# Kernel optimization log

Measured on AMD Instinct MI355X. Metric: run time of the kernel, lower is better.

## Reference

```python
import jax, jax.numpy as jnp
import numpy as np

N = 50000
NEG_SLOPE = 0.2


def add_self_loops(edge_index, n):
    loop = jnp.arange(n, dtype=edge_index.dtype)
    return jnp.concatenate([edge_index, jnp.stack([loop, loop])], axis=1)


def gatv2_conv(x, edge_index, Wl, bl, Wr, br, att, bias):
    """PyG GATv2Conv (share_weights=False, concat=True, add_self_loops applied by caller).
    x: [N, Fin]; edge_index: [2, E] with row0=src(j), row1=dst(i); att: [H, D].
    Returns (out [N, H*D], alpha [E, H])."""
    src, dst = edge_index[0], edge_index[1]
    H, D = att.shape
    n = x.shape[0]
    xl = (x @ Wl + bl).reshape(n, H, D)   # source-side transform
    xr = (x @ Wr + br).reshape(n, H, D)   # target-side transform
    e = jax.nn.leaky_relu(xl[src] + xr[dst], NEG_SLOPE)        # [E, H, D]
    logit = jnp.einsum('ehd,hd->eh', e, att)                    # [E, H]
    # segment softmax over edges grouped by target node
    lmax = jax.ops.segment_max(logit, dst, num_segments=n)      # [N, H]
    ex = jnp.exp(logit - lmax[dst])
    denom = jax.ops.segment_sum(ex, dst, num_segments=n)
    alpha = ex / denom[dst]                                     # [E, H]
    out = jax.ops.segment_sum(alpha[:, :, None] * xl[src], dst, num_segments=n)  # [N, H, D]
    return out.reshape(n, H * D) + bias, alpha


def setup_inputs() -> dict:
    key = jax.random.key(0)
    ks = jax.random.split(key, 16)
    E = 400000
    x = jax.random.normal(ks[0], (N, 23), dtype=jnp.float32)
    edge_index = jax.random.randint(ks[1], (2, E), 0, N, dtype=jnp.int64)
    H1, D1 = 8, 64
    F1 = H1 * D1  # 512
    s = 0.1
    return {
        'x': x,
        'edge_index': edge_index,
        'Wl1': jax.random.normal(ks[2], (23, F1), dtype=jnp.float32) * s,
        'bl1': jnp.zeros((F1,), jnp.float32),
        'Wr1': jax.random.normal(ks[3], (23, F1), dtype=jnp.float32) * s,
        'br1': jnp.zeros((F1,), jnp.float32),
        'att1': jax.random.normal(ks[4], (H1, D1), dtype=jnp.float32) * s,
        'bias1': jnp.zeros((F1,), jnp.float32),
        'Wl2': jax.random.normal(ks[5], (F1, 1), dtype=jnp.float32) * s,
        'bl2': jnp.zeros((1,), jnp.float32),
        'Wr2': jax.random.normal(ks[6], (F1, 1), dtype=jnp.float32) * s,
        'br2': jnp.zeros((1,), jnp.float32),
        'att2': jax.random.normal(ks[7], (1, 1), dtype=jnp.float32) * s,
        'bias2': jnp.zeros((1,), jnp.float32),
    }


def reference(x, edge_index, Wl1, bl1, Wr1, br1, att1, bias1,
              Wl2, bl2, Wr2, br2, att2, bias2):
    ei = add_self_loops(edge_index, N)
    h, _ = gatv2_conv(x, ei, Wl1, bl1, Wr1, br1, att1, bias1)
    h = jax.nn.relu(h)
    h, alpha = gatv2_conv(h, ei, Wl2, bl2, Wr2, br2, att2, bias2)
    return h, alpha
```

## Files before the change

kernel.cpp:

```cpp
#include <hip/hip_runtime.h>
#include <math.h>

#define NN 50000
#define E0 400000
#define EE 450000
#define FF 512
#define G1 2048
#define NPB 25
#define EPB 220
#define WAVES_TOTAL (G1 * 4)
#define MAXD 64
#define LOG2E 1.44269504f

typedef _Float16 h2 __attribute__((ext_vector_type(2)));

__device__ __forceinline__ h2 uas_h2(unsigned u) { union { unsigned u; h2 h; } c; c.u = u; return c.h; }
__device__ __forceinline__ unsigned h2as_u(h2 h) { union { unsigned u; h2 h; } c; c.h = h; return c.u; }
__device__ __forceinline__ unsigned packh(float a, float b) {
    h2 hh = { (_Float16)a, (_Float16)b };
    return h2as_u(hh);
}
__device__ __forceinline__ float leaky(float v) { return fmaxf(v, 0.2f * v); }

template <int CTRL>
__device__ __forceinline__ float dpp_add(float v) {
    int x = __builtin_bit_cast(int, v);
    int y = __builtin_amdgcn_update_dpp(0, x, CTRL, 0xF, 0xF, true);
    return v + __builtin_bit_cast(float, y);
}

__global__ __launch_bounds__(256) void k_predeg(
    const float* __restrict__ x,
    const float* __restrict__ Wl1, const float* __restrict__ bl1,
    const float* __restrict__ Wr1, const float* __restrict__ br1,
    const int* __restrict__ ei,
    unsigned* __restrict__ xlh, unsigned* __restrict__ xrh,
    int* __restrict__ cnt, int* __restrict__ src_sl)
{
    __shared__ unsigned sxh[NPB * 12];
    int b = blockIdx.x, t = threadIdx.x;

    int e0 = b * EPB;
    int e1 = e0 + EPB; if (e1 > EE) e1 = EE;
    int e = e0 + t;
    int esrc = 0, edst = -1;
    if (e < e1) {
        if (e < E0) { esrc = ei[e]; edst = ei[E0 + e]; }
        else        { esrc = e - E0; edst = esrc; }
    }

    int i0 = b * NPB;
    int i1 = i0 + NPB; if (i1 > NN) i1 = NN;
    int nnod = i1 - i0;
    for (int k = t; k < nnod * 12; k += 256) {
        int n = k / 12, j = k - n * 12;
        const float* row = x + (size_t)(i0 + n) * 23;
        float f0 = row[2 * j];
        float f1 = (2 * j + 1 < 23) ? row[2 * j + 1] : 0.f;
        sxh[n * 12 + j] = packh(f0, f1);
    }

    int c0 = 2 * t, c1 = 2 * t + 1;
    h2 wl0[12], wl1v[12], wr0[12], wr1v[12];
#pragma unroll
    for (int j = 0; j < 12; j++) {
        int r0 = 2 * j, r1 = 2 * j + 1;
        float a, b2;
        a = Wl1[r0 * FF + c0]; b2 = (r1 < 23) ? Wl1[r1 * FF + c0] : 0.f;
        wl0[j] = (h2){ (_Float16)a, (_Float16)b2 };
        a = Wl1[r0 * FF + c1]; b2 = (r1 < 23) ? Wl1[r1 * FF + c1] : 0.f;
        wl1v[j] = (h2){ (_Float16)a, (_Float16)b2 };
        a = Wr1[r0 * FF + c0]; b2 = (r1 < 23) ? Wr1[r1 * FF + c0] : 0.f;
        wr0[j] = (h2){ (_Float16)a, (_Float16)b2 };
        a = Wr1[r0 * FF + c1]; b2 = (r1 < 23) ? Wr1[r1 * FF + c1] : 0.f;
        wr1v[j] = (h2){ (_Float16)a, (_Float16)b2 };
    }
    float bl0 = bl1[c0], bl1s = bl1[c1];
    float br0 = br1[c0], br1s = br1[c1];
    __syncthreads();

    const uint4* S = (const uint4*)sxh;
    uint4 xa = S[0], xb = S[1], xc = S[2];
    for (int n = 0; n < nnod; n++) {
        uint4 na = xa, nb = xb, nc = xc;
        if (n + 1 < nnod) {
            na = S[(n + 1) * 3 + 0];
            nb = S[(n + 1) * 3 + 1];
            nc = S[(n + 1) * 3 + 2];
        }
        h2 xv[12] = { uas_h2(xa.x), uas_h2(xa.y), uas_h2(xa.z), uas_h2(xa.w),
                      uas_h2(xb.x), uas_h2(xb.y), uas_h2(xb.z), uas_h2(xb.w),
                      uas_h2(xc.x), uas_h2(xc.y), uas_h2(xc.z), uas_h2(xc.w) };
        float al0 = bl0, al1 = bl1s, ar0 = br0, ar1 = br1s;
#pragma unroll
        for (int j = 0; j < 12; j++) {
            al0 = __builtin_amdgcn_fdot2(wl0[j], xv[j], al0, false);
            al1 = __builtin_amdgcn_fdot2(wl1v[j], xv[j], al1, false);
            ar0 = __builtin_amdgcn_fdot2(wr0[j], xv[j], ar0, false);
            ar1 = __builtin_amdgcn_fdot2(wr1v[j], xv[j], ar1, false);
        }
        xlh[(size_t)(i0 + n) * 256 + t] = packh(al0, al1);
        xrh[(size_t)(i0 + n) * 256 + t] = packh(ar0, ar1);
        xa = na; xb = nb; xc = nc;
    }

    if (edst >= 0) {
        int p = atomicAdd(&cnt[edst], 1);
        if (p < MAXD) src_sl[(size_t)edst * MAXD + p] = esrc;
    }
}

__global__ __launch_bounds__(256) void k_layer1(
    const uint4* __restrict__ xlh, const uint4* __restrict__ xrh,
    const float* __restrict__ att, const float* __restrict__ bias1,
    const float* __restrict__ Wl2, const float* __restrict__ bl2,
    const float* __restrict__ Wr2, const float* __restrict__ br2,
    const int* __restrict__ cnt, const int* __restrict__ src_sl,
    float* __restrict__ xl2, float* __restrict__ xr2)
{
    int t = threadIdx.x;
    int l = t & 63;
    int wid = blockIdx.x * 4 + (t >> 6);

    float4 atA = ((const float4*)att)[2 * l];
    float4 atB = ((const float4*)att)[2 * l + 1];
    h2 a6_0 = { (_Float16)(0.6f * LOG2E * atA.x), (_Float16)(0.6f * LOG2E * atA.y) };
    h2 a6_1 = { (_Float16)(0.6f * LOG2E * atA.z), (_Float16)(0.6f * LOG2E * atA.w) };
    h2 a6_2 = { (_Float16)(0.6f * LOG2E * atB.x), (_Float16)(0.6f * LOG2E * atB.y) };
    h2 a6_3 = { (_Float16)(0.6f * LOG2E * atB.z), (_Float16)(0.6f * LOG2E * atB.w) };
    h2 a4_0 = { (_Float16)(0.4f * LOG2E * atA.x), (_Float16)(0.4f * LOG2E * atA.y) };
    h2 a4_1 = { (_Float16)(0.4f * LOG2E * atA.z), (_Float16)(0.4f * LOG2E * atA.w) };
    h2 a4_2 = { (_Float16)(0.4f * LOG2E * atB.x), (_Float16)(0.4f * LOG2E * atB.y) };
    h2 a4_3 = { (_Float16)(0.4f * LOG2E * atB.z), (_Float16)(0.4f * LOG2E * atB.w) };
    float bl2v = bl2[0], br2v = br2[0];

    int i = wid;
    int dg0 = 0, myj = 0; uint4 xq = {0, 0, 0, 0};
    if (i < NN) {
        dg0 = cnt[i];
        myj = src_sl[(size_t)i * MAXD + l];
        xq  = xrh[(size_t)i * 64 + l];
    }

    for (; i < NN; i += WAVES_TOTAL) {
        int dg = dg0; if (dg > MAXD) dg = MAXD;

        int s0 = 0;
        int s1 = (dg > 1) ? 1 : 0;
        int s2 = (dg > 2) ? 2 : s1;
        int s3 = (dg > 3) ? 3 : s2;
        uint4 ra = xlh[(size_t)__builtin_amdgcn_readlane(myj, s0) * 64 + l];
        uint4 rb = xlh[(size_t)__builtin_amdgcn_readlane(myj, s1) * 64 + l];
        uint4 rc = xlh[(size_t)__builtin_amdgcn_readlane(myj, s2) * 64 + l];
        uint4 rd = xlh[(size_t)__builtin_amdgcn_readlane(myj, s3) * 64 + l];

        int inext = i + WAVES_TOTAL;
        int dg_n = 0, myj_n = 0; uint4 xq_n = {0, 0, 0, 0};
        if (inext < NN) {
            dg_n  = cnt[inext];
            myj_n = src_sl[(size_t)inext * MAXD + l];
            xq_n  = xrh[(size_t)inext * 64 + l];
        }

        h2 q0 = uas_h2(xq.x), q1 = uas_h2(xq.y), q2 = uas_h2(xq.z), q3 = uas_h2(xq.w);

        float s = 0.f;
        h2 A0 = { 0, 0 }, A1 = { 0, 0 }, A2 = { 0, 0 }, A3 = { 0, 0 };

#define PROC(RV)                                                               \
        {                                                                      \
            h2 p0 = uas_h2(RV.x), p1 = uas_h2(RV.y),                           \
               p2 = uas_h2(RV.z), p3 = uas_h2(RV.w);                           \
            h2 t0 = p0 + q0, t1 = p1 + q1, t2 = p2 + q2, t3 = p3 + q3;         \
            h2 b0 = uas_h2(h2as_u(t0) & 0x7fff7fffu);                          \
            h2 b1 = uas_h2(h2as_u(t1) & 0x7fff7fffu);                          \
            h2 b2 = uas_h2(h2as_u(t2) & 0x7fff7fffu);                          \
            h2 b3 = uas_h2(h2as_u(t3) & 0x7fff7fffu);                          \
            float part = 0.f;                                                  \
            part = __builtin_amdgcn_fdot2(a6_0, t0, part, false);              \
            part = __builtin_amdgcn_fdot2(a4_0, b0, part, false);              \
            part = __builtin_amdgcn_fdot2(a6_1, t1, part, false);              \
            part = __builtin_amdgcn_fdot2(a4_1, b1, part, false);              \
            part = __builtin_amdgcn_fdot2(a6_2, t2, part, false);              \
            part = __builtin_amdgcn_fdot2(a4_2, b2, part, false);              \
            part = __builtin_amdgcn_fdot2(a6_3, t3, part, false);              \
            part = __builtin_amdgcn_fdot2(a4_3, b3, part, false);              \
            part = dpp_add<0xB1>(part);                                        \
            part = dpp_add<0x4E>(part);                                        \
            part = dpp_add<0x141>(part);                                       \
            float wv = exp2f(part);                                            \
            s += wv;                                                           \
            _Float16 wh = (_Float16)wv;                                        \
            h2 w2 = { wh, wh };                                                \
            A0 += w2 * p0;                                                     \
            A1 += w2 * p1;                                                     \
            A2 += w2 * p2;                                                     \
            A3 += w2 * p3;                                                     \
        }

        int p = 0;
        for (;;) {
            PROC(ra);
            if (++p >= dg) break;
            { int sl = p + 3 < dg ? p + 3 : dg - 1;
              ra = xlh[(size_t)__builtin_amdgcn_readlane(myj, sl) * 64 + l]; }
            PROC(rb);
            if (++p >= dg) break;
            { int sl = p + 3 < dg ? p + 3 : dg - 1;
              rb = xlh[(size_t)__builtin_amdgcn_readlane(myj, sl) * 64 + l]; }
            PROC(rc);
            if (++p >= dg) break;
            { int sl = p + 3 < dg ? p + 3 : dg - 1;
              rc = xlh[(size_t)__builtin_amdgcn_readlane(myj, sl) * 64 + l]; }
            PROC(rd);
            if (++p >= dg) break;
            { int sl = p + 3 < dg ? p + 3 : dg - 1;
              rd = xlh[(size_t)__builtin_amdgcn_readlane(myj, sl) * 64 + l]; }
        }
#undef PROC

        float inv = 1.f / s;
        float4 bA = ((const float4*)bias1)[2 * l];
        float4 bB = ((const float4*)bias1)[2 * l + 1];
        float h0 = fmaxf(fmaf((float)A0[0], inv, bA.x), 0.f);
        float h1 = fmaxf(fmaf((float)A0[1], inv, bA.y), 0.f);
        float h2v = fmaxf(fmaf((float)A1[0], inv, bA.z), 0.f);
        float h3 = fmaxf(fmaf((float)A1[1], inv, bA.w), 0.f);
        float h4 = fmaxf(fmaf((float)A2[0], inv, bB.x), 0.f);
        float h5 = fmaxf(fmaf((float)A2[1], inv, bB.y), 0.f);
        float h6 = fmaxf(fmaf((float)A3[0], inv, bB.z), 0.f);
        float h7 = fmaxf(fmaf((float)A3[1], inv, bB.w), 0.f);

        float4 wlA = ((const float4*)Wl2)[2 * l];
        float4 wlB = ((const float4*)Wl2)[2 * l + 1];
        float4 wrA = ((const float4*)Wr2)[2 * l];
        float4 wrB = ((const float4*)Wr2)[2 * l + 1];
        float pl = h0 * wlA.x + h1 * wlA.y + h2v * wlA.z + h3 * wlA.w
                 + h4 * wlB.x + h5 * wlB.y + h6 * wlB.z + h7 * wlB.w;
        float pr = h0 * wrA.x + h1 * wrA.y + h2v * wrA.z + h3 * wrA.w
                 + h4 * wrB.x + h5 * wrB.y + h6 * wrB.z + h7 * wrB.w;
#pragma unroll
        for (int o = 32; o > 0; o >>= 1) {
            pl += __shfl_xor(pl, o, 64);
            pr += __shfl_xor(pr, o, 64);
        }
        if (l == 0) {
            xl2[i] = pl + bl2v;
            xr2[i] = pr + br2v;
        }

        dg0 = dg_n; myj = myj_n; xq = xq_n;
    }
}

__global__ void k_layer2a(const float* __restrict__ xl2, const float* __restrict__ xr2,
                          const float* __restrict__ att2, const float* __restrict__ bias2,
                          const int* __restrict__ cnt, const int* __restrict__ src_sl,
                          float* __restrict__ out, float* __restrict__ invs)
{
    int i = blockIdx.x * blockDim.x + threadIdx.x;
    if (i >= NN) return;
    int dg = cnt[i]; if (dg > MAXD) dg = MAXD;
    const int* sp = src_sl + (size_t)i * MAXD;
    float xri = xr2[i];
    float a2l = att2[0] * LOG2E;
    float s = 0.f, num = 0.f;
    float va = xl2[sp[0]];
    float vb = (1 < dg) ? xl2[sp[1]] : 0.f;
    float vc = (2 < dg) ? xl2[sp[2]] : 0.f;
    float vd = (3 < dg) ? xl2[sp[3]] : 0.f;
    for (int p = 0; p < dg; p++) {
        float v = va; va = vb; vb = vc; vc = vd;
        vd = (p + 4 < dg) ? xl2[sp[p + 4]] : 0.f;
        float w = exp2f(leaky(v + xri) * a2l);
        s += w;
        num = fmaf(w, v, num);
    }
    out[i] = num / s + bias2[0];
    invs[i] = 1.f / s;
}

__global__ void k_layer2b(const float* __restrict__ xl2, const float* __restrict__ xr2,
                          const float* __restrict__ att2, const int* __restrict__ ei,
                          const float* __restrict__ invs, float* __restrict__ out)
{
    int e = blockIdx.x * blockDim.x + threadIdx.x;
    if (e >= EE) return;
    int src, dst;
    if (e < E0) { src = ei[e]; dst = ei[E0 + e]; }
    else        { src = e - E0; dst = src; }
    float a2l = att2[0] * LOG2E;
    float lg = leaky(xl2[src] + xr2[dst]) * a2l;
    out[NN + e] = exp2f(lg) * invs[dst];
}

extern "C" void kernel_launch(void* const* d_in, const int* in_sizes, int n_in,
                              void* d_out, int out_size, void* d_ws, size_t ws_size,
                              hipStream_t stream)
{
    const float* x     = (const float*)d_in[0];
    const int*   ei    = (const int*)d_in[1];
    const float* Wl1   = (const float*)d_in[2];
    const float* bl1   = (const float*)d_in[3];
    const float* Wr1   = (const float*)d_in[4];
    const float* br1   = (const float*)d_in[5];
    const float* att1  = (const float*)d_in[6];
    const float* bias1 = (const float*)d_in[7];
    const float* Wl2   = (const float*)d_in[8];
    const float* bl2   = (const float*)d_in[9];
    const float* Wr2   = (const float*)d_in[10];
    const float* br2   = (const float*)d_in[11];
    const float* att2  = (const float*)d_in[12];
    const float* bias2 = (const float*)d_in[13];
    float* out = (float*)d_out;

    char* ws = (char*)d_ws;
    unsigned* xlh  = (unsigned*)ws; ws += (size_t)NN * 256 * 4;
    unsigned* xrh  = (unsigned*)ws; ws += (size_t)NN * 256 * 4;
    float* xl2     = (float*)ws;    ws += (size_t)NN * 4;
    float* xr2     = (float*)ws;    ws += (size_t)NN * 4;
    float* invs    = (float*)ws;    ws += (size_t)NN * 4;
    int* cnt       = (int*)ws;      ws += (size_t)NN * 4;
    int* src_sl    = (int*)ws;      ws += (size_t)NN * MAXD * 4;

    (void)hipMemsetAsync(cnt, 0, (size_t)NN * 4, stream);

    k_predeg<<<G1, 256, 0, stream>>>(x, Wl1, bl1, Wr1, br1, ei, xlh, xrh,
                                     cnt, src_sl);
    k_layer1<<<G1, 256, 0, stream>>>((const uint4*)xlh, (const uint4*)xrh,
                                     att1, bias1, Wl2, bl2, Wr2, br2,
                                     cnt, src_sl, xl2, xr2);
    k_layer2a<<<(NN + 255) / 256, 256, 0, stream>>>(xl2, xr2, att2, bias2,
                                                    cnt, src_sl, out, invs);
    k_layer2b<<<(EE + 255) / 256, 256, 0, stream>>>(xl2, xr2, att2, ei, invs, out);
}
```

Measured before the change: 213.8 us.

## Fuse scatter and both layers into one cooperative kernel with grid syncs

Moves the edge scatter out of the GEMM kernel and zeroes the counts inside the GEMM kernel in place of a memset. Scatter, layer-1 aggregation and both layer-2 passes now run in one cooperative persistent kernel separated by grid.sync, replacing three separate kernel launches. A non-cooperative multi-kernel fallback is used if occupancy is too low or the cooperative launch fails. This trades launch gaps and tail effects for grid-wide barriers and a smaller grid capped by occupancy (8 blocks per CU via launch bounds), which may add register pressure to the layer-1 phase.

```diff
diff --git a/kernel.cpp b/kernel.cpp
--- a/kernel.cpp
+++ b/kernel.cpp
@@ -1,5 +1,8 @@
 #include <hip/hip_runtime.h>
+#include <hip/hip_cooperative_groups.h>
 #include <math.h>
+
+namespace cg = cooperative_groups;
 
 #define NN 50000
 #define E0 400000
@@ -7,10 +10,9 @@
 #define FF 512
 #define G1 2048
 #define NPB 25
-#define EPB 220
-#define WAVES_TOTAL (G1 * 4)
 #define MAXD 64
 #define LOG2E 1.44269504f
+#define NCU 256
 
 typedef _Float16 h2 __attribute__((ext_vector_type(2)));
 
@@ -29,88 +31,22 @@
     return v + __builtin_bit_cast(float, y);
 }
 
-__global__ __launch_bounds__(256) void k_predeg(
-    const float* __restrict__ x,
-    const float* __restrict__ Wl1, const float* __restrict__ bl1,
-    const float* __restrict__ Wr1, const float* __restrict__ br1,
-    const int* __restrict__ ei,
-    unsigned* __restrict__ xlh, unsigned* __restrict__ xrh,
+
+__device__ __forceinline__ void phase_scatter(
+    int e0, int stride, const int* __restrict__ ei,
     int* __restrict__ cnt, int* __restrict__ src_sl)
 {
-    __shared__ unsigned sxh[NPB * 12];
-    int b = blockIdx.x, t = threadIdx.x;
-
-    int e0 = b * EPB;
-    int e1 = e0 + EPB; if (e1 > EE) e1 = EE;
-    int e = e0 + t;
-    int esrc = 0, edst = -1;
-    if (e < e1) {
-        if (e < E0) { esrc = ei[e]; edst = ei[E0 + e]; }
-        else        { esrc = e - E0; edst = esrc; }
-    }
-
-    int i0 = b * NPB;
-    int i1 = i0 + NPB; if (i1 > NN) i1 = NN;
-    int nnod = i1 - i0;
-    for (int k = t; k < nnod * 12; k += 256) {
-        int n = k / 12, j = k - n * 12;
-        const float* row = x + (size_t)(i0 + n) * 23;
-        float f0 = row[2 * j];
-        float f1 = (2 * j + 1 < 23) ? row[2 * j + 1] : 0.f;
-        sxh[n * 12 + j] = packh(f0, f1);
-    }
-
-    int c0 = 2 * t, c1 = 2 * t + 1;
-    h2 wl0[12], wl1v[12], wr0[12], wr1v[12];
-#pragma unroll
-    for (int j = 0; j < 12; j++) {
-        int r0 = 2 * j, r1 = 2 * j + 1;
-        float a, b2;
-        a = Wl1[r0 * FF + c0]; b2 = (r1 < 23) ? Wl1[r1 * FF + c0] : 0.f;
-        wl0[j] = (h2){ (_Float16)a, (_Float16)b2 };
-        a = Wl1[r0 * FF + c1]; b2 = (r1 < 23) ? Wl1[r1 * FF + c1] : 0.f;
-        wl1v[j] = (h2){ (_Float16)a, (_Float16)b2 };
-        a = Wr1[r0 * FF + c0]; b2 = (r1 < 23) ? Wr1[r1 * FF + c0] : 0.f;
-        wr0[j] = (h2){ (_Float16)a, (_Float16)b2 };
-        a = Wr1[r0 * FF + c1]; b2 = (r1 < 23) ? Wr1[r1 * FF + c1] : 0.f;
-        wr1v[j] = (h2){ (_Float16)a, (_Float16)b2 };
-    }
-    float bl0 = bl1[c0], bl1s = bl1[c1];
-    float br0 = br1[c0], br1s = br1[c1];
-    __syncthreads();
-
-    const uint4* S = (const uint4*)sxh;
-    uint4 xa = S[0], xb = S[1], xc = S[2];
-    for (int n = 0; n < nnod; n++) {
-        uint4 na = xa, nb = xb, nc = xc;
-        if (n + 1 < nnod) {
-            na = S[(n + 1) * 3 + 0];
-            nb = S[(n + 1) * 3 + 1];
-            nc = S[(n + 1) * 3 + 2];
-        }
-        h2 xv[12] = { uas_h2(xa.x), uas_h2(xa.y), uas_h2(xa.z), uas_h2(xa.w),
-                      uas_h2(xb.x), uas_h2(xb.y), uas_h2(xb.z), uas_h2(xb.w),
-                      uas_h2(xc.x), uas_h2(xc.y), uas_h2(xc.z), uas_h2(xc.w) };
-        float al0 = bl0, al1 = bl1s, ar0 = br0, ar1 = br1s;
-#pragma unroll
-        for (int j = 0; j < 12; j++) {
-            al0 = __builtin_amdgcn_fdot2(wl0[j], xv[j], al0, false);
-            al1 = __builtin_amdgcn_fdot2(wl1v[j], xv[j], al1, false);
-            ar0 = __builtin_amdgcn_fdot2(wr0[j], xv[j], ar0, false);
-            ar1 = __builtin_amdgcn_fdot2(wr1v[j], xv[j], ar1, false);
-        }
-        xlh[(size_t)(i0 + n) * 256 + t] = packh(al0, al1);
-        xrh[(size_t)(i0 + n) * 256 + t] = packh(ar0, ar1);
-        xa = na; xb = nb; xc = nc;
-    }
-
-    if (edst >= 0) {
-        int p = atomicAdd(&cnt[edst], 1);
-        if (p < MAXD) src_sl[(size_t)edst * MAXD + p] = esrc;
-    }
-}
-
-__global__ __launch_bounds__(256) void k_layer1(
+    for (int e = e0; e < EE; e += stride) {
+        int src, dst;
+        if (e < E0) { src = ei[e]; dst = ei[E0 + e]; }
+        else        { src = e - E0; dst = src; }
+        int p = atomicAdd(&cnt[dst], 1);
+        if (p < MAXD) src_sl[(size_t)dst * MAXD + p] = src;
+    }
+}
+
+__device__ __forceinline__ void phase_layer1(
+    int l, int wid, int wstep,
     const uint4* __restrict__ xlh, const uint4* __restrict__ xrh,
     const float* __restrict__ att, const float* __restrict__ bias1,
     const float* __restrict__ Wl2, const float* __restrict__ bl2,
@@ -118,10 +54,6 @@
     const int* __restrict__ cnt, const int* __restrict__ src_sl,
     float* __restrict__ xl2, float* __restrict__ xr2)
 {
-    int t = threadIdx.x;
-    int l = t & 63;
-    int wid = blockIdx.x * 4 + (t >> 6);
-
     float4 atA = ((const float4*)att)[2 * l];
     float4 atB = ((const float4*)att)[2 * l + 1];
     h2 a6_0 = { (_Float16)(0.6f * LOG2E * atA.x), (_Float16)(0.6f * LOG2E * atA.y) };
@@ -142,7 +74,7 @@
         xq  = xrh[(size_t)i * 64 + l];
     }
 
-    for (; i < NN; i += WAVES_TOTAL) {
+    for (; i < NN; i += wstep) {
         int dg = dg0; if (dg > MAXD) dg = MAXD;
 
         int s0 = 0;
@@ -154,7 +86,7 @@
         uint4 rc = xlh[(size_t)__builtin_amdgcn_readlane(myj, s2) * 64 + l];
         uint4 rd = xlh[(size_t)__builtin_amdgcn_readlane(myj, s3) * 64 + l];
 
-        int inext = i + WAVES_TOTAL;
+        int inext = i + wstep;
         int dg_n = 0, myj_n = 0; uint4 xq_n = {0, 0, 0, 0};
         if (inext < NN) {
             dg_n  = cnt[inext];
@@ -253,45 +185,185 @@
     }
 }
 
-__global__ void k_layer2a(const float* __restrict__ xl2, const float* __restrict__ xr2,
-                          const float* __restrict__ att2, const float* __restrict__ bias2,
-                          const int* __restrict__ cnt, const int* __restrict__ src_sl,
-                          float* __restrict__ out, float* __restrict__ invs)
-{
-    int i = blockIdx.x * blockDim.x + threadIdx.x;
-    if (i >= NN) return;
-    int dg = cnt[i]; if (dg > MAXD) dg = MAXD;
-    const int* sp = src_sl + (size_t)i * MAXD;
-    float xri = xr2[i];
-    float a2l = att2[0] * LOG2E;
-    float s = 0.f, num = 0.f;
-    float va = xl2[sp[0]];
-    float vb = (1 < dg) ? xl2[sp[1]] : 0.f;
-    float vc = (2 < dg) ? xl2[sp[2]] : 0.f;
-    float vd = (3 < dg) ? xl2[sp[3]] : 0.f;
-    for (int p = 0; p < dg; p++) {
-        float v = va; va = vb; vb = vc; vc = vd;
-        vd = (p + 4 < dg) ? xl2[sp[p + 4]] : 0.f;
-        float w = exp2f(leaky(v + xri) * a2l);
-        s += w;
-        num = fmaf(w, v, num);
-    }
-    out[i] = num / s + bias2[0];
-    invs[i] = 1.f / s;
-}
-
-__global__ void k_layer2b(const float* __restrict__ xl2, const float* __restrict__ xr2,
-                          const float* __restrict__ att2, const int* __restrict__ ei,
-                          const float* __restrict__ invs, float* __restrict__ out)
-{
-    int e = blockIdx.x * blockDim.x + threadIdx.x;
-    if (e >= EE) return;
-    int src, dst;
-    if (e < E0) { src = ei[e]; dst = ei[E0 + e]; }
-    else        { src = e - E0; dst = src; }
-    float a2l = att2[0] * LOG2E;
-    float lg = leaky(xl2[src] + xr2[dst]) * a2l;
-    out[NN + e] = exp2f(lg) * invs[dst];
+__device__ __forceinline__ void phase_l2a(
+    int i0, int stride,
+    const float* __restrict__ xl2, const float* __restrict__ xr2,
+    const float* __restrict__ att2, const float* __restrict__ bias2,
+    const int* __restrict__ cnt, const int* __restrict__ src_sl,
+    float* __restrict__ out, float* __restrict__ invs)
+{
+    for (int i = i0; i < NN; i += stride) {
+        int dg = cnt[i]; if (dg > MAXD) dg = MAXD;
+        const int* sp = src_sl + (size_t)i * MAXD;
+        float xri = xr2[i];
+        float a2l = att2[0] * LOG2E;
+        float s = 0.f, num = 0.f;
+        float va = xl2[sp[0]];
+        float vb = (1 < dg) ? xl2[sp[1]] : 0.f;
+        float vc = (2 < dg) ? xl2[sp[2]] : 0.f;
+        float vd = (3 < dg) ? xl2[sp[3]] : 0.f;
+        for (int p = 0; p < dg; p++) {
+            float v = va; va = vb; vb = vc; vc = vd;
+            vd = (p + 4 < dg) ? xl2[sp[p + 4]] : 0.f;
+            float w = exp2f(leaky(v + xri) * a2l);
+            s += w;
+            num = fmaf(w, v, num);
+        }
+        out[i] = num / s + bias2[0];
+        invs[i] = 1.f / s;
+    }
+}
+
+__device__ __forceinline__ void phase_l2b(
+    int e0, int stride,
+    const float* __restrict__ xl2, const float* __restrict__ xr2,
+    const float* __restrict__ att2, const int* __restrict__ ei,
+    const float* __restrict__ invs, float* __restrict__ out)
+{
+    for (int e = e0; e < EE; e += stride) {
+        int src, dst;
+        if (e < E0) { src = ei[e]; dst = ei[E0 + e]; }
+        else        { src = e - E0; dst = src; }
+        float a2l = att2[0] * LOG2E;
+        float lg = leaky(xl2[src] + xr2[dst]) * a2l;
+        out[NN + e] = exp2f(lg) * invs[dst];
+    }
+}
+
+
+__global__ __launch_bounds__(256) void k_pregemm(
+    const float* __restrict__ x,
+    const float* __restrict__ Wl1, const float* __restrict__ bl1,
+    const float* __restrict__ Wr1, const float* __restrict__ br1,
+    unsigned* __restrict__ xlh, unsigned* __restrict__ xrh,
+    int* __restrict__ cnt)
+{
+    __shared__ unsigned sxh[NPB * 12];
+    int b = blockIdx.x, t = threadIdx.x;
+
+    int z = b * 256 + t;
+    if (z < NN) cnt[z] = 0;
+
+    int i0 = b * NPB;
+    int i1 = i0 + NPB; if (i1 > NN) i1 = NN;
+    int nnod = i1 - i0;
+    for (int k = t; k < nnod * 12; k += 256) {
+        int n = k / 12, j = k - n * 12;
+        const float* row = x + (size_t)(i0 + n) * 23;
+        float f0 = row[2 * j];
+        float f1 = (2 * j + 1 < 23) ? row[2 * j + 1] : 0.f;
+        sxh[n * 12 + j] = packh(f0, f1);
+    }
+
+    int c0 = 2 * t, c1 = 2 * t + 1;
+    h2 wl0[12], wl1v[12], wr0[12], wr1v[12];
+#pragma unroll
+    for (int j = 0; j < 12; j++) {
+        int r0 = 2 * j, r1 = 2 * j + 1;
+        float a, b2;
+        a = Wl1[r0 * FF + c0]; b2 = (r1 < 23) ? Wl1[r1 * FF + c0] : 0.f;
+        wl0[j] = (h2){ (_Float16)a, (_Float16)b2 };
+        a = Wl1[r0 * FF + c1]; b2 = (r1 < 23) ? Wl1[r1 * FF + c1] : 0.f;
+        wl1v[j] = (h2){ (_Float16)a, (_Float16)b2 };
+        a = Wr1[r0 * FF + c0]; b2 = (r1 < 23) ? Wr1[r1 * FF + c0] : 0.f;
+        wr0[j] = (h2){ (_Float16)a, (_Float16)b2 };
+        a = Wr1[r0 * FF + c1]; b2 = (r1 < 23) ? Wr1[r1 * FF + c1] : 0.f;
+        wr1v[j] = (h2){ (_Float16)a, (_Float16)b2 };
+    }
+    float bl0 = bl1[c0], bl1s = bl1[c1];
+    float br0 = br1[c0], br1s = br1[c1];
+    __syncthreads();
+
+    const uint4* S = (const uint4*)sxh;
+    uint4 xa = S[0], xb = S[1], xc = S[2];
+    for (int n = 0; n < nnod; n++) {
+        uint4 na = xa, nb = xb, nc = xc;
+        if (n + 1 < nnod) {
+            na = S[(n + 1) * 3 + 0];
+            nb = S[(n + 1) * 3 + 1];
+            nc = S[(n + 1) * 3 + 2];
+        }
+        h2 xv[12] = { uas_h2(xa.x), uas_h2(xa.y), uas_h2(xa.z), uas_h2(xa.w),
+                      uas_h2(xb.x), uas_h2(xb.y), uas_h2(xb.z), uas_h2(xb.w),
+                      uas_h2(xc.x), uas_h2(xc.y), uas_h2(xc.z), uas_h2(xc.w) };
+        float al0 = bl0, al1 = bl1s, ar0 = br0, ar1 = br1s;
+#pragma unroll
+        for (int j = 0; j < 12; j++) {
+            al0 = __builtin_amdgcn_fdot2(wl0[j], xv[j], al0, false);
+            al1 = __builtin_amdgcn_fdot2(wl1v[j], xv[j], al1, false);
+            ar0 = __builtin_amdgcn_fdot2(wr0[j], xv[j], ar0, false);
+            ar1 = __builtin_amdgcn_fdot2(wr1v[j], xv[j], ar1, false);
+        }
+        xlh[(size_t)(i0 + n) * 256 + t] = packh(al0, al1);
+        xrh[(size_t)(i0 + n) * 256 + t] = packh(ar0, ar1);
+        xa = na; xb = nb; xc = nc;
+    }
+}
+
+__global__ __launch_bounds__(256, 8) void k_fused(
+    const uint4* __restrict__ xlh, const uint4* __restrict__ xrh,
+    const float* __restrict__ att, const float* __restrict__ bias1,
+    const float* __restrict__ Wl2, const float* __restrict__ bl2,
+    const float* __restrict__ Wr2, const float* __restrict__ br2,
+    int* __restrict__ cnt, int* __restrict__ src_sl,
+    float* __restrict__ xl2, float* __restrict__ xr2,
+    const int* __restrict__ ei,
+    const float* __restrict__ att2, const float* __restrict__ bias2,
+    float* __restrict__ out, float* __restrict__ invs)
+{
+    cg::grid_group grid = cg::this_grid();
+    int t = threadIdx.x;
+    int gtid = blockIdx.x * 256 + t;
+    int stride = gridDim.x * 256;
+
+    phase_scatter(gtid, stride, ei, cnt, src_sl);
+    grid.sync();
+    phase_layer1(t & 63, blockIdx.x * 4 + (t >> 6), gridDim.x * 4,
+                 xlh, xrh, att, bias1, Wl2, bl2, Wr2, br2,
+                 cnt, src_sl, xl2, xr2);
+    grid.sync();
+    phase_l2a(gtid, stride, xl2, xr2, att2, bias2, cnt, src_sl, out, invs);
+    grid.sync();
+    phase_l2b(gtid, stride, xl2, xr2, att2, ei, invs, out);
+}
+
+__global__ __launch_bounds__(256) void k_scatter(
+    const int* __restrict__ ei, int* __restrict__ cnt, int* __restrict__ src_sl)
+{
+    phase_scatter(blockIdx.x * 256 + threadIdx.x, gridDim.x * 256, ei, cnt, src_sl);
+}
+
+__global__ __launch_bounds__(256) void k_l1(
+    const uint4* __restrict__ xlh, const uint4* __restrict__ xrh,
+    const float* __restrict__ att, const float* __restrict__ bias1,
+    const float* __restrict__ Wl2, const float* __restrict__ bl2,
+    const float* __restrict__ Wr2, const float* __restrict__ br2,
+    const int* __restrict__ cnt, const int* __restrict__ src_sl,
+    float* __restrict__ xl2, float* __restrict__ xr2)
+{
+    int t = threadIdx.x;
+    phase_layer1(t & 63, blockIdx.x * 4 + (t >> 6), gridDim.x * 4,
+                 xlh, xrh, att, bias1, Wl2, bl2, Wr2, br2,
+                 cnt, src_sl, xl2, xr2);
+}
+
+__global__ __launch_bounds__(256) void k_l2a(
+    const float* __restrict__ xl2, const float* __restrict__ xr2,
+    const float* __restrict__ att2, const float* __restrict__ bias2,
+    const int* __restrict__ cnt, const int* __restrict__ src_sl,
+    float* __restrict__ out, float* __restrict__ invs)
+{
+    phase_l2a(blockIdx.x * 256 + threadIdx.x, gridDim.x * 256,
+              xl2, xr2, att2, bias2, cnt, src_sl, out, invs);
+}
+
+__global__ __launch_bounds__(256) void k_l2b(
+    const float* __restrict__ xl2, const float* __restrict__ xr2,
+    const float* __restrict__ att2, const int* __restrict__ ei,
+    const float* __restrict__ invs, float* __restrict__ out)
+{
+    phase_l2b(blockIdx.x * 256 + threadIdx.x, gridDim.x * 256,
+              xl2, xr2, att2, ei, invs, out);
 }
 
 extern "C" void kernel_launch(void* const* d_in, const int* in_sizes, int n_in,
@@ -312,7 +384,7 @@
     const float* br2   = (const float*)d_in[11];
     const float* att2  = (const float*)d_in[12];
     const float* bias2 = (const float*)d_in[13];
-    float* out = (float*)d_out;
+    float* outp = (float*)d_out;
 
     char* ws = (char*)d_ws;
     unsigned* xlh  = (unsigned*)ws; ws += (size_t)NN * 256 * 4;
@@ -323,14 +395,40 @@
     int* cnt       = (int*)ws;      ws += (size_t)NN * 4;
     int* src_sl    = (int*)ws;      ws += (size_t)NN * MAXD * 4;
 
-    (void)hipMemsetAsync(cnt, 0, (size_t)NN * 4, stream);
-
-    k_predeg<<<G1, 256, 0, stream>>>(x, Wl1, bl1, Wr1, br1, ei, xlh, xrh,
-                                     cnt, src_sl);
-    k_layer1<<<G1, 256, 0, stream>>>((const uint4*)xlh, (const uint4*)xrh,
-                                     att1, bias1, Wl2, bl2, Wr2, br2,
+    k_pregemm<<<G1, 256, 0, stream>>>(x, Wl1, bl1, Wr1, br1, xlh, xrh, cnt);
+
+    static int coopGrid = -1;
+    if (coopGrid < 0) {
+        int nb = 0;
+        if (hipOccupancyMaxActiveBlocksPerMultiprocessor(&nb, k_fused, 256, 0)
+                != hipSuccess)
+            nb = 0;
+        coopGrid = nb * NCU;
+        if (coopGrid > G1) coopGrid = G1;
+    }
+
+    const uint4* xlh4 = (const uint4*)xlh;
+    const uint4* xrh4 = (const uint4*)xrh;
+
+    bool done = false;
+    if (coopGrid >= 1536) {
+        void* kargs[] = {
+            (void*)&xlh4, (void*)&xrh4, (void*)&att1, (void*)&bias1,
+            (void*)&Wl2, (void*)&bl2, (void*)&Wr2, (void*)&br2,
+            (void*)&cnt, (void*)&src_sl, (void*)&xl2, (void*)&xr2,
+            (void*)&ei, (void*)&att2, (void*)&bias2,
+            (void*)&outp, (void*)&invs
+        };
+        if (hipLaunchCooperativeKernel((void*)k_fused, dim3(coopGrid), dim3(256),
+                                       kargs, 0, stream) == hipSuccess)
+            done = true;
+    }
+    if (!done) {
+        k_scatter<<<(EE + 255) / 256, 256, 0, stream>>>(ei, cnt, src_sl);
+        k_l1<<<G1, 256, 0, stream>>>(xlh4, xrh4, att1, bias1, Wl2, bl2, Wr2, br2,
                                      cnt, src_sl, xl2, xr2);
-    k_layer2a<<<(NN + 255) / 256, 256, 0, stream>>>(xl2, xr2, att2, bias2,
-                                                    cnt, src_sl, out, invs);
-    k_layer2b<<<(EE + 255) / 256, 256, 0, stream>>>(xl2, xr2, att2, ei, invs, out);
-}
+        k_l2a<<<(NN + 255) / 256, 256, 0, stream>>>(xl2, xr2, att2, bias2,
+                                                    cnt, src_sl, outp, invs);
+        k_l2b<<<(EE + 255) / 256, 256, 0, stream>>>(xl2, xr2, att2, ei, invs, outp);
+    }
+}
```

After: 228.3 us. 1.07x slower.

## Fuse layer-2 softmax and alpha output into one per-node kernel via edge ids

Applied to the files above, without the earlier changes.

Records each slotted edge's original edge id alongside its source in the bucketed adjacency during the degree pass. The layer-2 aggregation kernel then does a second pass over each node's bucket and writes the normalised alpha directly to the scattered edge positions. This removes the separate per-edge kernel and the invs buffer. In exchange it adds an extra scattered int write per edge in predeg, a second gather loop per node, and uncoalesced scattered stores of alpha.

```diff
diff --git a/kernel.cpp b/kernel.cpp
--- a/kernel.cpp
+++ b/kernel.cpp
@@ -35,7 +35,7 @@
     const float* __restrict__ Wr1, const float* __restrict__ br1,
     const int* __restrict__ ei,
     unsigned* __restrict__ xlh, unsigned* __restrict__ xrh,
-    int* __restrict__ cnt, int* __restrict__ src_sl)
+    int* __restrict__ cnt, int* __restrict__ src_sl, int* __restrict__ eid_sl)
 {
     __shared__ unsigned sxh[NPB * 12];
     int b = blockIdx.x, t = threadIdx.x;
@@ -106,7 +106,10 @@
 
     if (edst >= 0) {
         int p = atomicAdd(&cnt[edst], 1);
-        if (p < MAXD) src_sl[(size_t)edst * MAXD + p] = esrc;
+        if (p < MAXD) {
+            src_sl[(size_t)edst * MAXD + p] = esrc;
+            eid_sl[(size_t)edst * MAXD + p] = e;
+        }
     }
 }
 
@@ -253,15 +256,16 @@
     }
 }
 
-__global__ void k_layer2a(const float* __restrict__ xl2, const float* __restrict__ xr2,
-                          const float* __restrict__ att2, const float* __restrict__ bias2,
-                          const int* __restrict__ cnt, const int* __restrict__ src_sl,
-                          float* __restrict__ out, float* __restrict__ invs)
+__global__ void k_l2ab(const float* __restrict__ xl2, const float* __restrict__ xr2,
+                       const float* __restrict__ att2, const float* __restrict__ bias2,
+                       const int* __restrict__ cnt, const int* __restrict__ src_sl,
+                       const int* __restrict__ eid_sl, float* __restrict__ out)
 {
     int i = blockIdx.x * blockDim.x + threadIdx.x;
     if (i >= NN) return;
     int dg = cnt[i]; if (dg > MAXD) dg = MAXD;
     const int* sp = src_sl + (size_t)i * MAXD;
+    const int* ep = eid_sl + (size_t)i * MAXD;
     float xri = xr2[i];
     float a2l = att2[0] * LOG2E;
     float s = 0.f, num = 0.f;
@@ -277,21 +281,12 @@
         num = fmaf(w, v, num);
     }
     out[i] = num / s + bias2[0];
-    invs[i] = 1.f / s;
-}
-
-__global__ void k_layer2b(const float* __restrict__ xl2, const float* __restrict__ xr2,
-                          const float* __restrict__ att2, const int* __restrict__ ei,
-                          const float* __restrict__ invs, float* __restrict__ out)
-{
-    int e = blockIdx.x * blockDim.x + threadIdx.x;
-    if (e >= EE) return;
-    int src, dst;
-    if (e < E0) { src = ei[e]; dst = ei[E0 + e]; }
-    else        { src = e - E0; dst = src; }
-    float a2l = att2[0] * LOG2E;
-    float lg = leaky(xl2[src] + xr2[dst]) * a2l;
-    out[NN + e] = exp2f(lg) * invs[dst];
+    float inv = 1.f / s;
+    for (int p = 0; p < dg; p++) {
+        float v = xl2[sp[p]];
+        float w = exp2f(leaky(v + xri) * a2l);
+        out[NN + ep[p]] = w * inv;
+    }
 }
 
 extern "C" void kernel_launch(void* const* d_in, const int* in_sizes, int n_in,
@@ -319,18 +314,17 @@
     unsigned* xrh  = (unsigned*)ws; ws += (size_t)NN * 256 * 4;
     float* xl2     = (float*)ws;    ws += (size_t)NN * 4;
     float* xr2     = (float*)ws;    ws += (size_t)NN * 4;
-    float* invs    = (float*)ws;    ws += (size_t)NN * 4;
     int* cnt       = (int*)ws;      ws += (size_t)NN * 4;
     int* src_sl    = (int*)ws;      ws += (size_t)NN * MAXD * 4;
+    int* eid_sl    = (int*)ws;      ws += (size_t)NN * MAXD * 4;
 
     (void)hipMemsetAsync(cnt, 0, (size_t)NN * 4, stream);
 
     k_predeg<<<G1, 256, 0, stream>>>(x, Wl1, bl1, Wr1, br1, ei, xlh, xrh,
-                                     cnt, src_sl);
+                                     cnt, src_sl, eid_sl);
     k_layer1<<<G1, 256, 0, stream>>>((const uint4*)xlh, (const uint4*)xrh,
                                      att1, bias1, Wl2, bl2, Wr2, br2,
                                      cnt, src_sl, xl2, xr2);
-    k_layer2a<<<(NN + 255) / 256, 256, 0, stream>>>(xl2, xr2, att2, bias2,
-                                                    cnt, src_sl, out, invs);
-    k_layer2b<<<(EE + 255) / 256, 256, 0, stream>>>(xl2, xr2, att2, ei, invs, out);
-}
+    k_l2ab<<<(NN + 255) / 256, 256, 0, stream>>>(xl2, xr2, att2, bias2,
+                                                 cnt, src_sl, eid_sl, out);
+}
```

Measured after the change: 222.8 us. 1.04x slower.
